# Optimization experiments

Measured on AMD Instinct MI355X. Metric: run time of the kernel, lower is better.

The kernel has to match this reference:

```python
import jax, jax.numpy as jnp
import numpy as np

B, T, H = 2, 2048, 1024
DFF = 4 * H        # dense_mlp hidden width
E = 8              # num_experts_temp
TOP_K = 2


def setup_inputs() -> dict:
    key = jax.random.key(0)
    ks = jax.random.split(key, 6)
    s_h = 1.0 / np.sqrt(H)
    s_f = 1.0 / np.sqrt(DFF)
    return {
        "hidden_states": jax.random.normal(ks[0], (B, T, H), dtype=jnp.float32),
        "router_w": jax.random.normal(ks[1], (E, H), dtype=jnp.float32) * s_h,
        "w1": jax.random.normal(ks[2], (E, H, DFF), dtype=jnp.float32) * s_h,
        "b1": jnp.zeros((E, DFF), dtype=jnp.float32),
        "w2": jax.random.normal(ks[3], (E, DFF, H), dtype=jnp.float32) * s_f,
        "b2": jnp.zeros((E, H), dtype=jnp.float32),
    }


def reference(hidden_states, router_w, w1, b1, w2, b2):
    # Router: [B,T,E]
    router_logits = jnp.einsum("bth,eh->bte", hidden_states, router_w)
    topk_vals, topk_idx = jax.lax.top_k(router_logits, TOP_K)        # [B,T,K]
    topk_w = jax.nn.softmax(topk_vals.astype(jnp.float32), axis=-1)
    topk_w = topk_w.astype(hidden_states.dtype)

    # Dense compute of ALL experts (faithful to the original module).
    h = jnp.einsum("bth,ehf->btef", hidden_states, w1) + b1          # [B,T,E,DFF]
    h = jax.nn.gelu(h)
    expert_out = jnp.einsum("btef,efh->bteh", h, w2) + b2            # [B,T,E,H]

    # Gather top-k experts per token and mix.
    topk_out = jnp.take_along_axis(expert_out, topk_idx[..., None], axis=2)  # [B,T,K,H]
    mixed = jnp.sum(topk_out * topk_w[..., None], axis=2)            # [B,T,H]
    return mixed
```

## Files before the change

### kernel.cpp

```cpp
#include <hip/hip_runtime.h>
#include <hip/hip_bf16.h>
#include <stdint.h>

#define AS1 __attribute__((address_space(1)))
#define AS3 __attribute__((address_space(3)))

typedef __bf16 bf16x8 __attribute__((ext_vector_type(8)));
typedef float floatx4 __attribute__((ext_vector_type(4)));

static constexpr int NTOK = 4096;
static constexpr int H    = 1024;
static constexpr int DFF  = 4096;
static constexpr int E    = 8;
static constexpr int BN   = 128;
static constexpr int RBMAX = 72;

static constexpr size_t OFF_WS     = 0;
static constexpr size_t OFF_XCS    = 67108864;
static constexpr size_t OFF_HS     = 85983232;
static constexpr size_t OFF_P1     = 161480704;
static constexpr size_t OFF_RTIDX  = 180355072;
static constexpr size_t OFF_RTW    = 180387840;
static constexpr size_t OFF_PTOK   = 180420608;
static constexpr size_t OFF_PW     = 180457472;
static constexpr size_t OFF_TOKPOS = 180494336;
static constexpr size_t OFF_CNT    = 180527104;
static constexpr size_t WS_NEED    = 180527232;

__device__ __forceinline__ unsigned short f2bf(float f) {
    __bf16 b = (__bf16)f;
    return __builtin_bit_cast(unsigned short, b);
}
__device__ __forceinline__ float bf2f(unsigned short u) {
    unsigned int v = ((unsigned int)u) << 16;
    return __builtin_bit_cast(float, v);
}

__device__ __forceinline__ void gload16(const void* g, void* l) {
    __builtin_amdgcn_global_load_lds((AS1 void*)g, (AS3 void*)l, 16, 0, 0);
}

__global__ __launch_bounds__(256) void k_router(const float* __restrict__ x,
                                                const float* __restrict__ rw,
                                                int* __restrict__ rt_idx,
                                                float* __restrict__ rt_w,
                                                int* __restrict__ counts) {
    const int wv = threadIdx.x >> 6, ln = threadIdx.x & 63;
    const int t = blockIdx.x * 4 + wv;
    const float* xr = x + (size_t)t * H + ln * 4;
    float4 xv[4];
#pragma unroll
    for (int c = 0; c < 4; ++c) xv[c] = *(const float4*)(xr + c * 256);
    float lg[E];
#pragma unroll
    for (int e = 0; e < E; ++e) {
        const float* rr = rw + (size_t)e * H + ln * 4;
        float acc = 0.f;
#pragma unroll
        for (int c = 0; c < 4; ++c) {
            float4 rv = *(const float4*)(rr + c * 256);
            acc += xv[c].x * rv.x + xv[c].y * rv.y + xv[c].z * rv.z + xv[c].w * rv.w;
        }
#pragma unroll
        for (int s = 32; s > 0; s >>= 1) acc += __shfl_xor(acc, s, 64);
        lg[e] = acc;
    }
    if (ln == 0) {
        int i0 = 0; float v0 = lg[0];
#pragma unroll
        for (int e = 1; e < E; ++e) if (lg[e] > v0) { v0 = lg[e]; i0 = e; }
        int i1 = -1; float v1 = -INFINITY;
#pragma unroll
        for (int e = 0; e < E; ++e) if (e != i0 && lg[e] > v1) { v1 = lg[e]; i1 = e; }
        float e1 = expf(v1 - v0);
        float inv = 1.f / (1.f + e1);
        rt_idx[2 * t] = i0; rt_idx[2 * t + 1] = i1;
        rt_w[2 * t] = inv;  rt_w[2 * t + 1] = e1 * inv;
        atomicAdd(&counts[i0], 1);
        atomicAdd(&counts[i1], 1);
    }
}

__global__ void k_offsets(const int* __restrict__ counts, int* __restrict__ offs) {
    if (threadIdx.x == 0) {
        int o = 0;
        for (int e = 0; e < E; ++e) { offs[e] = o; o += (counts[e] + 127) & ~127; }
        offs[E] = o;
    }
}

__global__ __launch_bounds__(256) void k_scatter(const int* __restrict__ rt_idx,
                                                 const float* __restrict__ rt_w,
                                                 const int* __restrict__ offs,
                                                 int* __restrict__ cursors,
                                                 int* __restrict__ pair_tok,
                                                 float* __restrict__ pair_w,
                                                 int* __restrict__ tok_pos) {
    int t = blockIdx.x * 256 + threadIdx.x;
    if (t >= NTOK) return;
    for (int k = 0; k < 2; ++k) {
        int e = rt_idx[2 * t + k];
        int p = atomicAdd(&cursors[e], 1);
        int pos = offs[e] + p;
        pair_tok[pos] = t;
        pair_w[pos] = rt_w[2 * t + k];
        tok_pos[2 * t + k] = pos;
    }
}

__global__ __launch_bounds__(256) void k_gather(const float* __restrict__ x,
                                                const int* __restrict__ offs,
                                                const int* __restrict__ counts,
                                                const int* __restrict__ pair_tok,
                                                unsigned short* __restrict__ xcs) {
    int pos = blockIdx.x;
    if (pos >= offs[E]) return;
    int e = 0;
    while (e < E - 1 && pos >= offs[e + 1]) ++e;
    bool valid = (pos - offs[e]) < counts[e];
    int tok = valid ? pair_tok[pos] : 0;
    int k0 = threadIdx.x * 4;
    float4 xv = valid ? *(const float4*)(x + (size_t)tok * H + k0)
                      : make_float4(0.f, 0.f, 0.f, 0.f);
    ushort4 o;
    o.x = f2bf(xv.x); o.y = f2bf(xv.y); o.z = f2bf(xv.z); o.w = f2bf(xv.w);
    int rb = pos >> 7, m = pos & 127;
    size_t idx = (((size_t)(rb * 32 + (k0 >> 5)) * 128 + m) * 32) + (((k0 >> 3) & 3) << 3) + (k0 & 7);
    *(ushort4*)(xcs + idx) = o;
}

template <int K, int N>
__global__ __launch_bounds__(256) void k_convert(const float* __restrict__ w,
                                                 unsigned short* __restrict__ ws) {
    constexpr int KB = K / 32, NB = N / 64;
    int bid = blockIdx.x;
    int nb = bid % NB, kb = (bid / NB) % KB, e = bid / (NB * KB);
    int kq = threadIdx.x & 3, nl = threadIdx.x >> 2;
    int n = nb * 64 + nl;
    const float* src = w + ((size_t)e * K + kb * 32 + kq * 8) * N + n;
    union { unsigned short us[8]; uint4 v; } u;
#pragma unroll
    for (int j = 0; j < 8; ++j) u.us[j] = f2bf(src[(size_t)j * N]);
    size_t oct = ((size_t)(e * KB + kb) * N + n) * 4 + kq;
    *(uint4*)(ws + oct * 8) = u.v;
}

__global__ __launch_bounds__(256) void k_gemm1(const unsigned short* __restrict__ Xc,
                                               const unsigned short* __restrict__ W1s,
                                               const int* __restrict__ offs,
                                               const float* __restrict__ b1,
                                               unsigned short* __restrict__ Hs) {
    constexpr int KB = H / 32;
    constexpr int MP = 36;
    const int rb = blockIdx.y;
    if (rb * 128 >= offs[E]) return;
    int e = 0;
    while (e < E - 1 && rb * 128 >= offs[e + 1]) ++e;
    const int n0 = blockIdx.x * BN;

    __shared__ unsigned short smem[4 * 128 * MP];
    unsigned short* lds_a = smem;
    unsigned short* lds_b = smem + 4096;

    const int tid = threadIdx.x;
    const int wv = tid >> 6, ln = tid & 63;
    const int quad = ln >> 4, lr = ln & 15;
    const int wm = (wv & 1) * 64, wn = (wv >> 1) * 64;

    floatx4 acc[4][4];
#pragma unroll
    for (int i = 0; i < 4; ++i)
#pragma unroll
        for (int j = 0; j < 4; ++j) acc[i][j] = (floatx4){0.f, 0.f, 0.f, 0.f};

    const unsigned short* Atile = Xc + (size_t)rb * KB * 4096;
    const unsigned short* Btile = W1s + ((size_t)e * KB * DFF + n0) * 32;

    for (int kb = 0; kb < KB; ++kb) {
        __syncthreads();
        const unsigned short* a_src = Atile + (size_t)kb * 4096 + (wv * 2) * 512 + ln * 8;
        const unsigned short* b_src = Btile + (size_t)kb * DFF * 32 + (wv * 2) * 512 + ln * 8;
#pragma unroll
        for (int c = 0; c < 2; ++c) {
            gload16(a_src + c * 512, &lds_a[(wv * 2 + c) * 512]);
            gload16(b_src + c * 512, &lds_b[(wv * 2 + c) * 512]);
        }
        __syncthreads();
        bf16x8 af[4], bg[4];
#pragma unroll
        for (int i = 0; i < 4; ++i) {
            af[i] = *(const bf16x8*)(lds_a + (wm + i * 16 + lr) * 32 + quad * 8);
            bg[i] = *(const bf16x8*)(lds_b + (wn + i * 16 + lr) * 32 + quad * 8);
        }
#pragma unroll
        for (int i = 0; i < 4; ++i)
#pragma unroll
            for (int j = 0; j < 4; ++j)
                acc[i][j] = __builtin_amdgcn_mfma_f32_16x16x32_bf16(af[i], bg[j], acc[i][j], 0, 0, 0);
    }

    float bj[4];
#pragma unroll
    for (int j = 0; j < 4; ++j) bj[j] = b1[(size_t)e * DFF + n0 + wn + j * 16 + lr];
    __syncthreads();
#pragma unroll
    for (int j = 0; j < 4; ++j) {
        const int fl = wn + j * 16 + lr;
        const int fb = fl >> 5, f5 = fl & 31;
        unsigned short* dst = smem + fb * (128 * MP) + f5;
#pragma unroll
        for (int i = 0; i < 4; ++i) {
#pragma unroll
            for (int r = 0; r < 4; ++r) {
                const int m = wm + i * 16 + quad * 4 + r;
                float v = acc[i][j][r] + bj[j];
                float u = 0.79788456080286535588f * (v + 0.044715f * v * v * v);
                float ez = __expf(2.f * u);
                float g = v * (1.f - 1.f / (ez + 1.f));
                dst[m * MP] = f2bf(g);
            }
        }
    }
    __syncthreads();
    const size_t hsbase = ((size_t)rb * 128 + (n0 >> 5)) * 4096;
#pragma unroll
    for (int it = 0; it < 8; ++it) {
        const int g = (it * 256 + tid) * 8;
        const int fb = g >> 12, rem = g & 4095, m = rem >> 5, f5 = rem & 31;
        const unsigned short* s = smem + fb * (128 * MP) + m * MP + f5;
        uint2 lo = *(const uint2*)s;
        uint2 hi = *(const uint2*)(s + 4);
        *(uint4*)(Hs + hsbase + (size_t)g) = make_uint4(lo.x, lo.y, hi.x, hi.y);
    }
}

__global__ __launch_bounds__(256) void k_gemm2(const unsigned short* __restrict__ Hs,
                                               const unsigned short* __restrict__ W2s,
                                               const int* __restrict__ offs,
                                               const float* __restrict__ b2,
                                               unsigned short* __restrict__ P0,
                                               unsigned short* __restrict__ P1) {
    constexpr int KB = DFF / 32;
    constexpr int KBS = KB / 2;
    const int rb = blockIdx.y;
    if (rb * 128 >= offs[E]) return;
    int e = 0;
    while (e < E - 1 && rb * 128 >= offs[e + 1]) ++e;
    const int ks = blockIdx.z;
    const int n0 = blockIdx.x * BN;

    __shared__ unsigned short smem[8192];
    unsigned short* lds_a = smem;
    unsigned short* lds_b = smem + 4096;

    const int tid = threadIdx.x;
    const int wv = tid >> 6, ln = tid & 63;
    const int quad = ln >> 4, lr = ln & 15;
    const int wm = (wv & 1) * 64, wn = (wv >> 1) * 64;

    floatx4 acc[4][4];
#pragma unroll
    for (int i = 0; i < 4; ++i)
#pragma unroll
        for (int j = 0; j < 4; ++j) acc[i][j] = (floatx4){0.f, 0.f, 0.f, 0.f};

    const unsigned short* Atile = Hs + (size_t)rb * KB * 4096;
    const unsigned short* Btile = W2s + ((size_t)e * KB * H + n0) * 32;

    for (int kb = ks * KBS; kb < ks * KBS + KBS; ++kb) {
        __syncthreads();
        const unsigned short* a_src = Atile + (size_t)kb * 4096 + (wv * 2) * 512 + ln * 8;
        const unsigned short* b_src = Btile + (size_t)kb * H * 32 + (wv * 2) * 512 + ln * 8;
#pragma unroll
        for (int c = 0; c < 2; ++c) {
            gload16(a_src + c * 512, &lds_a[(wv * 2 + c) * 512]);
            gload16(b_src + c * 512, &lds_b[(wv * 2 + c) * 512]);
        }
        __syncthreads();
        bf16x8 af[4], bg[4];
#pragma unroll
        for (int i = 0; i < 4; ++i) {
            af[i] = *(const bf16x8*)(lds_a + (wm + i * 16 + lr) * 32 + quad * 8);
            bg[i] = *(const bf16x8*)(lds_b + (wn + i * 16 + lr) * 32 + quad * 8);
        }
#pragma unroll
        for (int i = 0; i < 4; ++i)
#pragma unroll
            for (int j = 0; j < 4; ++j)
                acc[i][j] = __builtin_amdgcn_mfma_f32_16x16x32_bf16(af[i], bg[j], acc[i][j], 0, 0, 0);
    }

    float bj[4];
#pragma unroll
    for (int j = 0; j < 4; ++j)
        bj[j] = (ks == 0) ? b2[(size_t)e * H + n0 + wn + j * 16 + lr] : 0.f;
    unsigned short* P = ks ? P1 : P0;
#pragma unroll
    for (int i = 0; i < 4; ++i) {
#pragma unroll
        for (int r = 0; r < 4; ++r) {
            const int m = wm + i * 16 + quad * 4 + r;
            unsigned short* row = P + (size_t)(rb * 128 + m) * H + n0;
#pragma unroll
            for (int j = 0; j < 4; ++j)
                row[wn + j * 16 + lr] = f2bf(acc[i][j][r] + bj[j]);
        }
    }
}

__global__ __launch_bounds__(256) void k_mix(const unsigned short* __restrict__ P0,
                                             const unsigned short* __restrict__ P1,
                                             const int* __restrict__ tok_pos,
                                             const float* __restrict__ rt_w,
                                             float* __restrict__ out) {
    const int t = blockIdx.x;
    const int c = threadIdx.x * 4;
    const int p0 = tok_pos[2 * t], p1 = tok_pos[2 * t + 1];
    const float w0 = rt_w[2 * t], w1 = rt_w[2 * t + 1];
    ushort4 a0 = *(const ushort4*)(P0 + (size_t)p0 * H + c);
    ushort4 a1 = *(const ushort4*)(P1 + (size_t)p0 * H + c);
    ushort4 b0 = *(const ushort4*)(P0 + (size_t)p1 * H + c);
    ushort4 b1 = *(const ushort4*)(P1 + (size_t)p1 * H + c);
    float4 o;
    o.x = w0 * (bf2f(a0.x) + bf2f(a1.x)) + w1 * (bf2f(b0.x) + bf2f(b1.x));
    o.y = w0 * (bf2f(a0.y) + bf2f(a1.y)) + w1 * (bf2f(b0.y) + bf2f(b1.y));
    o.z = w0 * (bf2f(a0.z) + bf2f(a1.z)) + w1 * (bf2f(b0.z) + bf2f(b1.z));
    o.w = w0 * (bf2f(a0.w) + bf2f(a1.w)) + w1 * (bf2f(b0.w) + bf2f(b1.w));
    *(float4*)(out + (size_t)t * H + c) = o;
}

extern "C" void kernel_launch(void* const* d_in, const int* in_sizes, int n_in,
                              void* d_out, int out_size, void* d_ws, size_t ws_size,
                              hipStream_t stream) {
    const float* x  = (const float*)d_in[0];
    const float* rw = (const float*)d_in[1];
    const float* w1 = (const float*)d_in[2];
    const float* b1 = (const float*)d_in[3];
    const float* w2 = (const float*)d_in[4];
    const float* b2 = (const float*)d_in[5];
    float* out = (float*)d_out;
    char* ws = (char*)d_ws;
    if (ws_size < WS_NEED) return;

    unsigned short* Ws   = (unsigned short*)(ws + OFF_WS);
    unsigned short* XcS  = (unsigned short*)(ws + OFF_XCS);
    unsigned short* Hs   = (unsigned short*)(ws + OFF_HS);
    unsigned short* P1   = (unsigned short*)(ws + OFF_P1);
    int*   rt_idx   = (int*)(ws + OFF_RTIDX);
    float* rt_w     = (float*)(ws + OFF_RTW);
    int*   pair_tok = (int*)(ws + OFF_PTOK);
    float* pair_w   = (float*)(ws + OFF_PW);
    int*   tok_pos  = (int*)(ws + OFF_TOKPOS);
    int*   cnt      = (int*)(ws + OFF_CNT);
    int*   cur      = cnt + 8;
    int*   offs     = cnt + 16;

    hipMemsetAsync(cnt, 0, 128, stream);

    k_router<<<NTOK / 4, 256, 0, stream>>>(x, rw, rt_idx, rt_w, cnt);
    k_offsets<<<1, 64, 0, stream>>>(cnt, offs);
    k_scatter<<<NTOK / 256, 256, 0, stream>>>(rt_idx, rt_w, offs, cur, pair_tok, pair_w, tok_pos);
    k_gather<<<9216, 256, 0, stream>>>(x, offs, cnt, pair_tok, XcS);

    k_convert<H, DFF><<<8 * (H / 32) * (DFF / 64), 256, 0, stream>>>(w1, Ws);
    k_gemm1<<<dim3(DFF / BN, RBMAX), 256, 0, stream>>>(XcS, Ws, offs, b1, Hs);

    k_convert<DFF, H><<<8 * (DFF / 32) * (H / 64), 256, 0, stream>>>(w2, Ws);
    k_gemm2<<<dim3(H / BN, RBMAX, 2), 256, 0, stream>>>(Hs, Ws, offs, b2, XcS, P1);

    k_mix<<<NTOK, 256, 0, stream>>>(XcS, P1, tok_pos, rt_w, out);
}
```

Measured before the change: 689.9 us.

## Coalesce weight conversion via LDS transpose and swizzle GEMM blocks across XCDs

```diff
diff --git a/kernel.cpp b/kernel.cpp
--- a/kernel.cpp
+++ b/kernel.cpp
@@ -132,17 +132,31 @@
 template <int K, int N>
 __global__ __launch_bounds__(256) void k_convert(const float* __restrict__ w,
                                                  unsigned short* __restrict__ ws) {
-    constexpr int KB = K / 32, NB = N / 64;
-    int bid = blockIdx.x;
-    int nb = bid % NB, kb = (bid / NB) % KB, e = bid / (NB * KB);
-    int kq = threadIdx.x & 3, nl = threadIdx.x >> 2;
-    int n = nb * 64 + nl;
-    const float* src = w + ((size_t)e * K + kb * 32 + kq * 8) * N + n;
-    union { unsigned short us[8]; uint4 v; } u;
-#pragma unroll
-    for (int j = 0; j < 8; ++j) u.us[j] = f2bf(src[(size_t)j * N]);
-    size_t oct = ((size_t)(e * KB + kb) * N + n) * 4 + kq;
-    *(uint4*)(ws + oct * 8) = u.v;
+    constexpr int KB = K / 32, NC = N / 128;
+    const int bid = blockIdx.x;
+    const int nc = bid % NC, kb = (bid / NC) % KB, e = bid / (NC * KB);
+    const int n0 = nc * 128;
+    __shared__ float lp[32][128];
+    const int tid = threadIdx.x;
+    {
+        const int kr = tid >> 5;
+        const int c4 = (tid & 31) * 4;
+        const float* src = w + (size_t)(e * K + kb * 32 + kr) * N + n0 + c4;
+#pragma unroll
+        for (int c = 0; c < 4; ++c)
+            *(float4*)&lp[kr + 8 * c][c4] = *(const float4*)(src + (size_t)(8 * c) * N);
+    }
+    __syncthreads();
+    const size_t base = ((size_t)(e * KB + kb) * N + n0) * 4;
+#pragma unroll
+    for (int it = 0; it < 2; ++it) {
+        const int item = it * 256 + tid;
+        const int nl = item >> 2, kq = item & 3;
+        union { unsigned short us[8]; uint4 v; } u;
+#pragma unroll
+        for (int j = 0; j < 8; ++j) u.us[j] = f2bf(lp[kq * 8 + j][nl]);
+        *(uint4*)(ws + (base + (size_t)nl * 4 + kq) * 8) = u.v;
+    }
 }
 
 __global__ __launch_bounds__(256) void k_gemm1(const unsigned short* __restrict__ Xc,
@@ -152,11 +166,15 @@
                                                unsigned short* __restrict__ Hs) {
     constexpr int KB = H / 32;
     constexpr int MP = 36;
-    const int rb = blockIdx.y;
+    constexpr int NB = DFF / BN;
+    constexpr int CPX = NB * (RBMAX - 1) / 8;
+    const int bid = blockIdx.x;
+    const int t = (bid & 7) * CPX + (bid >> 3);
+    const int rb = t / NB;
     if (rb * 128 >= offs[E]) return;
     int e = 0;
     while (e < E - 1 && rb * 128 >= offs[e + 1]) ++e;
-    const int n0 = blockIdx.x * BN;
+    const int n0 = (t % NB) * BN;
 
     __shared__ unsigned short smem[4 * 128 * MP];
     unsigned short* lds_a = smem;
@@ -242,12 +260,17 @@
                                                unsigned short* __restrict__ P1) {
     constexpr int KB = DFF / 32;
     constexpr int KBS = KB / 2;
-    const int rb = blockIdx.y;
+    constexpr int NB = H / BN;
+    constexpr int CPX = NB * (RBMAX - 1) * 2 / 8;
+    const int bid = blockIdx.x;
+    const int t = (bid & 7) * CPX + (bid >> 3);
+    const int yz = t >> 3;
+    const int rb = yz % (RBMAX - 1);
+    const int ks = yz / (RBMAX - 1);
     if (rb * 128 >= offs[E]) return;
     int e = 0;
     while (e < E - 1 && rb * 128 >= offs[e + 1]) ++e;
-    const int ks = blockIdx.z;
-    const int n0 = blockIdx.x * BN;
+    const int n0 = (t & 7) * BN;
 
     __shared__ unsigned short smem[8192];
     unsigned short* lds_a = smem;
@@ -362,11 +385,11 @@
     k_scatter<<<NTOK / 256, 256, 0, stream>>>(rt_idx, rt_w, offs, cur, pair_tok, pair_w, tok_pos);
     k_gather<<<9216, 256, 0, stream>>>(x, offs, cnt, pair_tok, XcS);
 
-    k_convert<H, DFF><<<8 * (H / 32) * (DFF / 64), 256, 0, stream>>>(w1, Ws);
-    k_gemm1<<<dim3(DFF / BN, RBMAX), 256, 0, stream>>>(XcS, Ws, offs, b1, Hs);
-
-    k_convert<DFF, H><<<8 * (DFF / 32) * (H / 64), 256, 0, stream>>>(w2, Ws);
-    k_gemm2<<<dim3(H / BN, RBMAX, 2), 256, 0, stream>>>(Hs, Ws, offs, b2, XcS, P1);
+    k_convert<H, DFF><<<8 * (H / 32) * (DFF / 128), 256, 0, stream>>>(w1, Ws);
+    k_gemm1<<<32 * (RBMAX - 1), 256, 0, stream>>>(XcS, Ws, offs, b1, Hs);
+
+    k_convert<DFF, H><<<8 * (DFF / 32) * (H / 128), 256, 0, stream>>>(w2, Ws);
+    k_gemm2<<<8 * (RBMAX - 1) * 2, 256, 0, stream>>>(Hs, Ws, offs, b2, XcS, P1);
 
     k_mix<<<NTOK, 256, 0, stream>>>(XcS, P1, tok_pos, rt_w, out);
 }
```

After: 694.7 us. Within noise of the previous version (+0.7%).
